# Kernel tuning notes

Hardware: AMD Instinct MI355X
Metric: run time of the kernel (lower is better)

## Reference

```python
import jax, jax.numpy as jnp
import numpy as np

B, P, H, A = 256, 196, 1024, 512

def setup_inputs() -> dict:
    key = jax.random.key(0)
    ks = jax.random.split(key, 20)
    s = 1.0 / np.sqrt(H)
    sa = 1.0 / np.sqrt(A)
    return {
        "spatial_image": jax.random.normal(ks[0], (B, P, H), jnp.float32),
        "decoder_out": jax.random.normal(ks[1], (B, H), jnp.float32),
        "st": jax.random.normal(ks[2], (B, H), jnp.float32),
        "W_sen_aff": jax.random.uniform(ks[3], (H, H), jnp.float32, -s, s),
        "b_sen_aff": jax.random.uniform(ks[4], (H,), jnp.float32, -s, s),
        "W_sen_att": jax.random.uniform(ks[5], (H, A), jnp.float32, -s, s),
        "b_sen_att": jax.random.uniform(ks[6], (A,), jnp.float32, -s, s),
        "W_h_aff": jax.random.uniform(ks[7], (H, H), jnp.float32, -s, s),
        "b_h_aff": jax.random.uniform(ks[8], (H,), jnp.float32, -s, s),
        "W_h_att": jax.random.uniform(ks[9], (H, A), jnp.float32, -s, s),
        "b_h_att": jax.random.uniform(ks[10], (A,), jnp.float32, -s, s),
        "W_v_att": jax.random.uniform(ks[11], (H, A), jnp.float32, -s, s),
        "b_v_att": jax.random.uniform(ks[12], (A,), jnp.float32, -s, s),
        "W_alpha": jax.random.uniform(ks[13], (A, 1), jnp.float32, -sa, sa),
        "b_alpha": jax.random.uniform(ks[14], (1,), jnp.float32, -sa, sa),
        "W_ctx": jax.random.uniform(ks[15], (H, H), jnp.float32, -s, s),
        "b_ctx": jax.random.uniform(ks[16], (H,), jnp.float32, -s, s),
    }

def reference(spatial_image, decoder_out, st,
              W_sen_aff, b_sen_aff, W_sen_att, b_sen_att,
              W_h_aff, b_h_aff, W_h_att, b_h_att,
              W_v_att, b_v_att, W_alpha, b_alpha, W_ctx, b_ctx):
    # visual_attn: [B, P, A]
    visual_attn = jnp.einsum('bph,ha->bpa', spatial_image, W_v_att) + b_v_att
    # sentinel path: [B, H] -> relu affine -> [B, A]
    sentinel_affine = jax.nn.relu(st @ W_sen_aff + b_sen_aff)
    sentinel_attn = sentinel_affine @ W_sen_att + b_sen_att
    # hidden path: [B, H] -> tanh affine -> [B, A]
    hidden_affine = jnp.tanh(decoder_out @ W_h_aff + b_h_aff)
    hidden_attn = hidden_affine @ W_h_att + b_h_att
    # concat sentinel as an extra "pixel": [B, P+1, H] and [B, P+1, A]
    concat_features = jnp.concatenate([spatial_image, sentinel_affine[:, None, :]], axis=1)
    attended_features = jnp.concatenate([visual_attn, sentinel_attn[:, None, :]], axis=1)
    attention = jnp.tanh(attended_features + hidden_attn[:, None, :])  # [B, P+1, A]
    alpha = (jnp.einsum('bpa,ao->bpo', attention, W_alpha) + b_alpha)[..., 0]  # [B, P+1]
    att_weights = jax.nn.softmax(alpha, axis=1)
    context = jnp.einsum('bph,bp->bh', concat_features, att_weights)  # [B, H]
    beta_value = att_weights[:, -1:]  # [B, 1]
    out_l = jnp.tanh((context + hidden_affine) @ W_ctx + b_ctx)  # [B, H]
    return (out_l, att_weights, beta_value)
```

## Files before the change

kernel.cpp:

```cpp
#include <hip/hip_runtime.h>
#include <stdint.h>
#include <stddef.h>

typedef __attribute__((ext_vector_type(4))) float f32x4;
typedef __attribute__((ext_vector_type(8))) short short8;

#define MROWS 50176


static __device__ __forceinline__ int lds_off(int row, int k) {
    int slot = (k >> 3) ^ ((row >> 1) & 3);
    return (row << 6) + (slot << 4) + ((k & 7) << 1);
}

static __device__ __forceinline__ unsigned div196(unsigned g) {
    return (unsigned)(((unsigned long long)g * 85599ull) >> 24);
}

static __device__ __forceinline__ unsigned short f2bf(float f) {
    union { float f; unsigned u; } v; v.f = f;
    unsigned r = v.u + 0x7FFFu + ((v.u >> 16) & 1u);
    return (unsigned short)(r >> 16);
}

static __device__ __forceinline__ unsigned long long pack4bf(f32x4 a) {
    return  (unsigned long long)f2bf(a[0])
         | ((unsigned long long)f2bf(a[1]) << 16)
         | ((unsigned long long)f2bf(a[2]) << 32)
         | ((unsigned long long)f2bf(a[3]) << 48);
}

static __device__ __forceinline__ float tanh_fast(float x) {
    float xc = fminf(fmaxf(x, -9.f), 9.f);
    float e = __builtin_amdgcn_exp2f(xc * 2.885390081777927f);
    return (e - 1.f) * __builtin_amdgcn_rcpf(e + 1.f);
}

static __device__ __forceinline__ void gload_lds16(const void* g, void* l) {
    __builtin_amdgcn_global_load_lds(
        (const __attribute__((address_space(1))) unsigned int*)g,
        (__attribute__((address_space(3))) unsigned int*)l, 16, 0, 0);
}

static __device__ __forceinline__ void kloop_dbuf(
    const float* __restrict__ Abase,
    const unsigned short* __restrict__ Bbase,
    char* sA0, char* sA1, char* sB0, char* sB1,
    f32x4 acc[4][4], int tid)
{
    const int lane = tid & 63, w = tid >> 6;
    const int lrow = lane & 15, lk = lane >> 4;
    const int wr = w >> 1, wc = w & 1;

    const float* Ap[4];
    int aoff[4];
    #pragma unroll
    for (int r = 0; r < 4; ++r) {
        int q = tid + (r << 8);
        int ar = q >> 3, kc = (q & 7) << 2;
        Ap[r] = Abase + (size_t)ar * 1024 + kc;
        aoff[r] = lds_off(ar, kc);
    }
    const unsigned short* Bp[2];
    int bdst[2];
    #pragma unroll
    for (int c = 0; c < 2; ++c) {
        int ch = (w << 1) + c;
        int row = (ch << 4) + (lane >> 2);
        int kg = (lane & 3) ^ ((row >> 1) & 3);
        Bp[c] = Bbase + (size_t)row * 1024 + (kg << 3);
        bdst[c] = ch << 10;
    }

    f32x4 z = {0.f, 0.f, 0.f, 0.f};
    #pragma unroll
    for (int m = 0; m < 4; ++m)
        #pragma unroll
        for (int n = 0; n < 4; ++n) acc[m][n] = z;

    {
        f32x4 a[4];
        #pragma unroll
        for (int r = 0; r < 4; ++r) a[r] = *(const f32x4*)Ap[r];
        #pragma unroll
        for (int c = 0; c < 2; ++c) gload_lds16(Bp[c], sB0 + bdst[c]);
        #pragma unroll
        for (int r = 0; r < 4; ++r)
            *(unsigned long long*)(sA0 + aoff[r]) = pack4bf(a[r]);
    }
    __syncthreads();

    char* sAc = sA0; char* sAn = sA1;
    char* sBc = sB0; char* sBn = sB1;
    for (int ks = 0; ks < 32; ++ks) {
        f32x4 an[4];
        if (ks < 31) {
            const int ko = (ks + 1) << 5;
            #pragma unroll
            for (int r = 0; r < 4; ++r) an[r] = *(const f32x4*)(Ap[r] + ko);
            #pragma unroll
            for (int c = 0; c < 2; ++c) gload_lds16(Bp[c] + ko, sBn + bdst[c]);
        }
        short8 af[4], bf[4];
        #pragma unroll
        for (int m = 0; m < 4; ++m)
            af[m] = *(const short8*)(sAc + lds_off((wr << 6) + (m << 4) + lrow, lk << 3));
        #pragma unroll
        for (int n = 0; n < 4; ++n)
            bf[n] = *(const short8*)(sBc + lds_off((wc << 6) + (n << 4) + lrow, lk << 3));
        #pragma unroll
        for (int m = 0; m < 4; ++m)
            #pragma unroll
            for (int n = 0; n < 4; ++n)
                acc[m][n] = __builtin_amdgcn_mfma_f32_16x16x32_bf16(af[m], bf[n], acc[m][n], 0, 0, 0);
        if (ks < 31) {
            #pragma unroll
            for (int r = 0; r < 4; ++r)
                *(unsigned long long*)(sAn + aoff[r]) = pack4bf(an[r]);
        }
        __syncthreads();
        char* t;
        t = sAc; sAc = sAn; sAn = t;
        t = sBc; sBc = sBn; sBn = t;
    }
}

__global__ __launch_bounds__(256, 4) void attn_alpha_kernel(
    const float* __restrict__ spatial,
    const unsigned short* __restrict__ WvT,
    const float* __restrict__ b_v_att,
    const float* __restrict__ hidden_attn,
    const float* __restrict__ W_alpha,
    float* __restrict__ alphap)
{
    __shared__ char sA[2][8192];
    __shared__ char sB[2][8192];
    __shared__ float alpha_s[128];
    const int tid = threadIdx.x;
    const int n4 = blockIdx.x & 3, mt = blockIdx.x >> 2;
    const int row0 = mt << 7, col0 = n4 << 7;
    if (tid < 128) alpha_s[tid] = 0.f;

    f32x4 acc[4][4];
    kloop_dbuf(spatial + (size_t)row0 * 1024, WvT + (size_t)col0 * 1024,
               sA[0], sA[1], sB[0], sB[1], acc, tid);

    const int lane = tid & 63, w = tid >> 6;
    const int wr = w >> 1, wc = w & 1;
    const int lrow = lane & 15, lk = lane >> 4;

    const unsigned bb0 = div196((unsigned)row0);
    const unsigned bb1 = div196((unsigned)(row0 + 127));
    float bv[4], wa[4], h0[4], h1[4];
    #pragma unroll
    for (int n = 0; n < 4; ++n) {
        int g = col0 + (wc << 6) + (n << 4) + lrow;
        bv[n] = b_v_att[g];
        wa[n] = W_alpha[g];
        h0[n] = hidden_attn[bb0 * 512 + g];
        h1[n] = hidden_attn[bb1 * 512 + g];
    }
    #pragma unroll
    for (int m = 0; m < 4; ++m) {
        #pragma unroll
        for (int i = 0; i < 4; ++i) {
            int rloc = (wr << 6) + (m << 4) + (lk << 2) + i;
            bool first = (div196((unsigned)(row0 + rloc)) == bb0);
            float s = 0.f;
            #pragma unroll
            for (int n = 0; n < 4; ++n) {
                float v = tanh_fast(acc[m][n][i] + bv[n] + (first ? h0[n] : h1[n]));
                s += v * wa[n];
            }
            #pragma unroll
            for (int off = 1; off < 16; off <<= 1) s += __shfl_xor(s, off);
            if (lrow == 0) atomicAdd(&alpha_s[rloc], s);
        }
    }
    __syncthreads();
    if (tid < 128)
        alphap[(size_t)n4 * MROWS + row0 + tid] = alpha_s[tid];
}

struct GemmDesc { const float* A; const unsigned short* BT; const float* bias; float* C; int N; int act; };
struct GemmPair { GemmDesc d[2]; };

__global__ __launch_bounds__(256, 4) void gemm_pair_kernel(GemmPair p)
{
    GemmDesc d = p.d[blockIdx.z];
    __shared__ char sA[2][8192];
    __shared__ char sB[2][8192];
    const int tid = threadIdx.x;
    const int row0 = blockIdx.x << 7;
    const int col0 = blockIdx.y << 7;
    f32x4 acc[4][4];
    kloop_dbuf(d.A + (size_t)row0 * 1024, d.BT + (size_t)col0 * 1024,
               sA[0], sA[1], sB[0], sB[1], acc, tid);
    const int lane = tid & 63, w = tid >> 6;
    const int wr = w >> 1, wc = w & 1;
    const int lrow = lane & 15, lk = lane >> 4;
    #pragma unroll
    for (int n = 0; n < 4; ++n) {
        int col = col0 + (wc << 6) + (n << 4) + lrow;
        float bs = d.bias[col];
        #pragma unroll
        for (int m = 0; m < 4; ++m) {
            int rbase = row0 + (wr << 6) + (m << 4) + (lk << 2);
            #pragma unroll
            for (int i = 0; i < 4; ++i) {
                float v = acc[m][n][i] + bs;
                if (d.act == 1) v = fmaxf(v, 0.f);
                if (d.act == 2) v = tanh_fast(v);
                d.C[(size_t)(rbase + i) * d.N + col] = v;
            }
        }
    }
}

struct TransDesc { const float* src; unsigned short* dst; int K; int N; };
struct TransArgs { TransDesc d[6]; };

__global__ void transpose_cvt_kernel(TransArgs args) {
    TransDesc d = args.d[blockIdx.y];
    int nt = d.N >> 5;
    int tiles = (d.K >> 5) * nt;
    if ((int)blockIdx.x >= tiles) return;
    int tk = blockIdx.x / nt, tn = blockIdx.x % nt;
    __shared__ unsigned short tile[32][33];
    int tx = threadIdx.x & 31, ty = threadIdx.x >> 5;
    int k0 = tk << 5, n0 = tn << 5;
    #pragma unroll
    for (int j = 0; j < 4; ++j)
        tile[ty + j * 8][tx] = f2bf(d.src[(size_t)(k0 + ty + j * 8) * d.N + n0 + tx]);
    __syncthreads();
    #pragma unroll
    for (int j = 0; j < 4; ++j)
        d.dst[(size_t)(n0 + ty + j * 8) * d.K + k0 + tx] = tile[tx][ty + j * 8];
}

__global__ void softmax_sentinel_kernel(
    const float* __restrict__ alphap,
    const float* __restrict__ sen_att, const float* __restrict__ hid_att,
    const float* __restrict__ W_alpha,
    float* __restrict__ att, float* __restrict__ beta)
{
    int b = blockIdx.x, tid = threadIdx.x;
    __shared__ float al[197];
    __shared__ float red[4];
    if (tid < 196) {
        size_t g = (size_t)b * 196 + tid;
        al[tid] = alphap[g] + alphap[MROWS + g] + alphap[2 * MROWS + g] + alphap[3 * MROWS + g];
    }
    float s = 0.f;
    for (int a = tid; a < 512; a += 256)
        s += tanh_fast(sen_att[b * 512 + a] + hid_att[b * 512 + a]) * W_alpha[a];
    #pragma unroll
    for (int off = 1; off < 64; off <<= 1) s += __shfl_xor(s, off);
    if ((tid & 63) == 0) red[tid >> 6] = s;
    __syncthreads();
    if (tid == 0) al[196] = red[0] + red[1] + red[2] + red[3];
    __syncthreads();
    if (tid < 64) {
        float v[4];
        float mx = -1e30f;
        #pragma unroll
        for (int j = 0; j < 4; ++j) {
            int i = tid + j * 64;
            v[j] = (i < 197) ? al[i] : -1e30f;
            mx = fmaxf(mx, v[j]);
        }
        #pragma unroll
        for (int off = 1; off < 64; off <<= 1) mx = fmaxf(mx, __shfl_xor(mx, off));
        float sm = 0.f;
        #pragma unroll
        for (int j = 0; j < 4; ++j) {
            v[j] = __builtin_amdgcn_exp2f((v[j] - mx) * 1.442695040888963f);
            if (tid + j * 64 >= 197) v[j] = 0.f;
            sm += v[j];
        }
        #pragma unroll
        for (int off = 1; off < 64; off <<= 1) sm += __shfl_xor(sm, off);
        float inv = 1.f / sm;
        #pragma unroll
        for (int j = 0; j < 4; ++j) {
            int i = tid + j * 64;
            if (i < 197) {
                float wv = v[j] * inv;
                att[b * 197 + i] = wv;
                if (i == 196) beta[b] = wv;
            }
        }
    }
}

__global__ __launch_bounds__(256) void context_kernel(
    const float* __restrict__ spatial, const float* __restrict__ sen_aff,
    const float* __restrict__ hid_aff, const float* __restrict__ att,
    float* __restrict__ ctxh)
{
    int b = blockIdx.x, half = blockIdx.y, t = threadIdx.x;
    __shared__ float wsm[197];
    if (t < 197) wsm[t] = att[b * 197 + t];
    __syncthreads();
    int h2 = (half << 8) + t;
    const float2* sp = (const float2*)(spatial + (size_t)b * 196 * 1024) + h2;
    float ax = 0.f, ay = 0.f;
    #pragma unroll 4
    for (int p = 0; p < 196; ++p) {
        float2 x = sp[(size_t)p * 512];
        ax += wsm[p] * x.x; ay += wsm[p] * x.y;
    }
    float w196 = wsm[196];
    float2 sa = ((const float2*)(sen_aff + (size_t)b * 1024))[h2];
    float2 ha = ((const float2*)(hid_aff + (size_t)b * 1024))[h2];
    ctxh[(size_t)b * 1024 + 2 * h2]     = ax + w196 * sa.x + ha.x;
    ctxh[(size_t)b * 1024 + 2 * h2 + 1] = ay + w196 * sa.y + ha.y;
}

extern "C" void kernel_launch(void* const* d_in, const int* in_sizes, int n_in,
                              void* d_out, int out_size, void* d_ws, size_t ws_size,
                              hipStream_t stream)
{
    const float* spatial   = (const float*)d_in[0];
    const float* decoder   = (const float*)d_in[1];
    const float* st        = (const float*)d_in[2];
    const float* W_sen_aff = (const float*)d_in[3];
    const float* b_sen_aff = (const float*)d_in[4];
    const float* W_sen_att = (const float*)d_in[5];
    const float* b_sen_att = (const float*)d_in[6];
    const float* W_h_aff   = (const float*)d_in[7];
    const float* b_h_aff   = (const float*)d_in[8];
    const float* W_h_att   = (const float*)d_in[9];
    const float* b_h_att   = (const float*)d_in[10];
    const float* W_v_att   = (const float*)d_in[11];
    const float* b_v_att   = (const float*)d_in[12];
    const float* W_alpha   = (const float*)d_in[13];
    const float* W_ctx     = (const float*)d_in[15];
    const float* b_ctx     = (const float*)d_in[16];

    char* ws = (char*)d_ws;
    size_t off = 0;
    auto alloc = [&](size_t bytes) {
        char* p = ws + off; off += (bytes + 255) & ~(size_t)255; return p;
    };
    unsigned short* WvT  = (unsigned short*)alloc((size_t)512 * 1024 * 2);
    unsigned short* WsaT = (unsigned short*)alloc((size_t)1024 * 1024 * 2);
    unsigned short* WstT = (unsigned short*)alloc((size_t)512 * 1024 * 2);
    unsigned short* WhaT = (unsigned short*)alloc((size_t)1024 * 1024 * 2);
    unsigned short* WhtT = (unsigned short*)alloc((size_t)512 * 1024 * 2);
    unsigned short* WcxT = (unsigned short*)alloc((size_t)1024 * 1024 * 2);
    float* sen_aff = (float*)alloc((size_t)256 * 1024 * 4);
    float* sen_att = (float*)alloc((size_t)256 * 512 * 4);
    float* hid_aff = (float*)alloc((size_t)256 * 1024 * 4);
    float* hid_att = (float*)alloc((size_t)256 * 512 * 4);
    float* alphap  = (float*)alloc((size_t)4 * MROWS * 4);
    float* ctxh    = (float*)alloc((size_t)256 * 1024 * 4);

    float* out_l    = (float*)d_out;
    float* out_att  = out_l + 256 * 1024;
    float* out_beta = out_att + 256 * 197;

    TransArgs ta;
    ta.d[0] = { W_v_att,   WvT,  1024, 512  };
    ta.d[1] = { W_sen_aff, WsaT, 1024, 1024 };
    ta.d[2] = { W_sen_att, WstT, 1024, 512  };
    ta.d[3] = { W_h_aff,   WhaT, 1024, 1024 };
    ta.d[4] = { W_h_att,   WhtT, 1024, 512  };
    ta.d[5] = { W_ctx,     WcxT, 1024, 1024 };
    transpose_cvt_kernel<<<dim3(1024, 6), 256, 0, stream>>>(ta);

    GemmPair p1;
    p1.d[0] = { st,      WsaT, b_sen_aff, sen_aff, 1024, 1 };
    p1.d[1] = { decoder, WhaT, b_h_aff,   hid_aff, 1024, 2 };
    gemm_pair_kernel<<<dim3(2, 8, 2), 256, 0, stream>>>(p1);

    GemmPair p2;
    p2.d[0] = { sen_aff, WstT, b_sen_att, sen_att, 512, 0 };
    p2.d[1] = { hid_aff, WhtT, b_h_att,   hid_att, 512, 0 };
    gemm_pair_kernel<<<dim3(2, 4, 2), 256, 0, stream>>>(p2);

    attn_alpha_kernel<<<1568, 256, 0, stream>>>(spatial, WvT, b_v_att, hid_att, W_alpha, alphap);
    softmax_sentinel_kernel<<<256, 256, 0, stream>>>(alphap, sen_att, hid_att, W_alpha, out_att, out_beta);
    context_kernel<<<dim3(256, 2), 256, 0, stream>>>(spatial, sen_aff, hid_aff, out_att, ctxh);

    GemmPair p3;
    p3.d[0] = { ctxh, WcxT, b_ctx, out_l, 1024, 2 };
    p3.d[1] = { ctxh, WcxT, b_ctx, out_l, 1024, 2 };
    gemm_pair_kernel<<<dim3(2, 8, 1), 256, 0, stream>>>(p3);
}
```

Baseline: 248.2 us.

## Stream GEMM operands directly from global memory into MFMA fragments, dropping LDS staging

Replaces the LDS double-buffered K loop with a loop where each lane loads its A rows (fp32, converted to bf16) and B rows straight from global memory into MFMA fragments. This removes all barriers and LDS traffic. Each block's A/B tiles are re-read by multiple waves through cache instead of being shared via LDS. The change also remaps the block order of the attention GEMM so adjacent blocks are spread across XCDs, lowers launch bounds to 3 blocks per CU, and raises the unroll factor of the context reduction loop. The risk is more global and L2 traffic, plus uncoalesced, strided 32-byte row loads.

```diff
diff --git a/kernel.cpp b/kernel.cpp
--- a/kernel.cpp
+++ b/kernel.cpp
@@ -1,4 +1,5 @@
 #include <hip/hip_runtime.h>
+#include <hip/hip_bf16.h>
 #include <stdint.h>
 #include <stddef.h>
 
@@ -7,11 +8,6 @@
 
 #define MROWS 50176
 
-
-static __device__ __forceinline__ int lds_off(int row, int k) {
-    int slot = (k >> 3) ^ ((row >> 1) & 3);
-    return (row << 6) + (slot << 4) + ((k & 7) << 1);
-}
 
 static __device__ __forceinline__ unsigned div196(unsigned g) {
     return (unsigned)(((unsigned long long)g * 85599ull) >> 24);
@@ -23,54 +19,38 @@
     return (unsigned short)(r >> 16);
 }
 
-static __device__ __forceinline__ unsigned long long pack4bf(f32x4 a) {
-    return  (unsigned long long)f2bf(a[0])
-         | ((unsigned long long)f2bf(a[1]) << 16)
-         | ((unsigned long long)f2bf(a[2]) << 32)
-         | ((unsigned long long)f2bf(a[3]) << 48);
-}
-
 static __device__ __forceinline__ float tanh_fast(float x) {
     float xc = fminf(fmaxf(x, -9.f), 9.f);
     float e = __builtin_amdgcn_exp2f(xc * 2.885390081777927f);
     return (e - 1.f) * __builtin_amdgcn_rcpf(e + 1.f);
 }
 
-static __device__ __forceinline__ void gload_lds16(const void* g, void* l) {
-    __builtin_amdgcn_global_load_lds(
-        (const __attribute__((address_space(1))) unsigned int*)g,
-        (__attribute__((address_space(3))) unsigned int*)l, 16, 0, 0);
-}
-
-static __device__ __forceinline__ void kloop_dbuf(
-    const float* __restrict__ Abase,
-    const unsigned short* __restrict__ Bbase,
-    char* sA0, char* sA1, char* sB0, char* sB1,
+static __device__ __forceinline__ short8 cvt8bf(f32x4 lo, f32x4 hi) {
+    union { short8 s; __hip_bfloat162 h[4]; } u;
+    u.h[0] = __float22bfloat162_rn(make_float2(lo[0], lo[1]));
+    u.h[1] = __float22bfloat162_rn(make_float2(lo[2], lo[3]));
+    u.h[2] = __float22bfloat162_rn(make_float2(hi[0], hi[1]));
+    u.h[3] = __float22bfloat162_rn(make_float2(hi[2], hi[3]));
+    return u.s;
+}
+
+static __device__ __forceinline__ void kloop_stream(
+    const float* __restrict__ A,
+    const unsigned short* __restrict__ B,
     f32x4 acc[4][4], int tid)
 {
     const int lane = tid & 63, w = tid >> 6;
+    const int wr = w >> 1, wc = w & 1;
     const int lrow = lane & 15, lk = lane >> 4;
-    const int wr = w >> 1, wc = w & 1;
 
     const float* Ap[4];
-    int aoff[4];
-    #pragma unroll
-    for (int r = 0; r < 4; ++r) {
-        int q = tid + (r << 8);
-        int ar = q >> 3, kc = (q & 7) << 2;
-        Ap[r] = Abase + (size_t)ar * 1024 + kc;
-        aoff[r] = lds_off(ar, kc);
-    }
-    const unsigned short* Bp[2];
-    int bdst[2];
-    #pragma unroll
-    for (int c = 0; c < 2; ++c) {
-        int ch = (w << 1) + c;
-        int row = (ch << 4) + (lane >> 2);
-        int kg = (lane & 3) ^ ((row >> 1) & 3);
-        Bp[c] = Bbase + (size_t)row * 1024 + (kg << 3);
-        bdst[c] = ch << 10;
-    }
+    const unsigned short* Bp[4];
+    #pragma unroll
+    for (int m = 0; m < 4; ++m)
+        Ap[m] = A + (size_t)((wr << 6) + (m << 4) + lrow) * 1024 + (lk << 3);
+    #pragma unroll
+    for (int n = 0; n < 4; ++n)
+        Bp[n] = B + (size_t)((wc << 6) + (n << 4) + lrow) * 1024 + (lk << 3);
 
     f32x4 z = {0.f, 0.f, 0.f, 0.f};
     #pragma unroll
@@ -78,54 +58,27 @@
         #pragma unroll
         for (int n = 0; n < 4; ++n) acc[m][n] = z;
 
-    {
-        f32x4 a[4];
-        #pragma unroll
-        for (int r = 0; r < 4; ++r) a[r] = *(const f32x4*)Ap[r];
-        #pragma unroll
-        for (int c = 0; c < 2; ++c) gload_lds16(Bp[c], sB0 + bdst[c]);
-        #pragma unroll
-        for (int r = 0; r < 4; ++r)
-            *(unsigned long long*)(sA0 + aoff[r]) = pack4bf(a[r]);
-    }
-    __syncthreads();
-
-    char* sAc = sA0; char* sAn = sA1;
-    char* sBc = sB0; char* sBn = sB1;
+    #pragma unroll 4
     for (int ks = 0; ks < 32; ++ks) {
-        f32x4 an[4];
-        if (ks < 31) {
-            const int ko = (ks + 1) << 5;
-            #pragma unroll
-            for (int r = 0; r < 4; ++r) an[r] = *(const f32x4*)(Ap[r] + ko);
-            #pragma unroll
-            for (int c = 0; c < 2; ++c) gload_lds16(Bp[c] + ko, sBn + bdst[c]);
-        }
         short8 af[4], bf[4];
         #pragma unroll
-        for (int m = 0; m < 4; ++m)
-            af[m] = *(const short8*)(sAc + lds_off((wr << 6) + (m << 4) + lrow, lk << 3));
+        for (int m = 0; m < 4; ++m) {
+            f32x4 lo = *(const f32x4*)(Ap[m] + (ks << 5));
+            f32x4 hi = *(const f32x4*)(Ap[m] + (ks << 5) + 4);
+            af[m] = cvt8bf(lo, hi);
+        }
         #pragma unroll
         for (int n = 0; n < 4; ++n)
-            bf[n] = *(const short8*)(sBc + lds_off((wc << 6) + (n << 4) + lrow, lk << 3));
+            bf[n] = *(const short8*)(Bp[n] + (ks << 5));
         #pragma unroll
         for (int m = 0; m < 4; ++m)
             #pragma unroll
             for (int n = 0; n < 4; ++n)
                 acc[m][n] = __builtin_amdgcn_mfma_f32_16x16x32_bf16(af[m], bf[n], acc[m][n], 0, 0, 0);
-        if (ks < 31) {
-            #pragma unroll
-            for (int r = 0; r < 4; ++r)
-                *(unsigned long long*)(sAn + aoff[r]) = pack4bf(an[r]);
-        }
-        __syncthreads();
-        char* t;
-        t = sAc; sAc = sAn; sAn = t;
-        t = sBc; sBc = sBn; sBn = t;
-    }
-}
-
-__global__ __launch_bounds__(256, 4) void attn_alpha_kernel(
+    }
+}
+
+__global__ __launch_bounds__(256, 3) void attn_alpha_kernel(
     const float* __restrict__ spatial,
     const unsigned short* __restrict__ WvT,
     const float* __restrict__ b_v_att,
@@ -133,17 +86,17 @@
     const float* __restrict__ W_alpha,
     float* __restrict__ alphap)
 {
-    __shared__ char sA[2][8192];
-    __shared__ char sB[2][8192];
     __shared__ float alpha_s[128];
     const int tid = threadIdx.x;
-    const int n4 = blockIdx.x & 3, mt = blockIdx.x >> 2;
+    const int j = blockIdx.x;
+    const int wk = (j & 7) * 196 + (j >> 3);
+    const int mt = wk >> 2, n4 = wk & 3;
     const int row0 = mt << 7, col0 = n4 << 7;
     if (tid < 128) alpha_s[tid] = 0.f;
+    __syncthreads();
 
     f32x4 acc[4][4];
-    kloop_dbuf(spatial + (size_t)row0 * 1024, WvT + (size_t)col0 * 1024,
-               sA[0], sA[1], sB[0], sB[1], acc, tid);
+    kloop_stream(spatial + (size_t)row0 * 1024, WvT + (size_t)col0 * 1024, acc, tid);
 
     const int lane = tid & 63, w = tid >> 6;
     const int wr = w >> 1, wc = w & 1;
@@ -185,17 +138,14 @@
 struct GemmDesc { const float* A; const unsigned short* BT; const float* bias; float* C; int N; int act; };
 struct GemmPair { GemmDesc d[2]; };
 
-__global__ __launch_bounds__(256, 4) void gemm_pair_kernel(GemmPair p)
+__global__ __launch_bounds__(256, 3) void gemm_pair_kernel(GemmPair p)
 {
     GemmDesc d = p.d[blockIdx.z];
-    __shared__ char sA[2][8192];
-    __shared__ char sB[2][8192];
     const int tid = threadIdx.x;
     const int row0 = blockIdx.x << 7;
     const int col0 = blockIdx.y << 7;
     f32x4 acc[4][4];
-    kloop_dbuf(d.A + (size_t)row0 * 1024, d.BT + (size_t)col0 * 1024,
-               sA[0], sA[1], sB[0], sB[1], acc, tid);
+    kloop_stream(d.A + (size_t)row0 * 1024, d.BT + (size_t)col0 * 1024, acc, tid);
     const int lane = tid & 63, w = tid >> 6;
     const int wr = w >> 1, wc = w & 1;
     const int lrow = lane & 15, lk = lane >> 4;
@@ -264,28 +214,28 @@
         float v[4];
         float mx = -1e30f;
         #pragma unroll
-        for (int j = 0; j < 4; ++j) {
-            int i = tid + j * 64;
-            v[j] = (i < 197) ? al[i] : -1e30f;
-            mx = fmaxf(mx, v[j]);
+        for (int jj = 0; jj < 4; ++jj) {
+            int i = tid + jj * 64;
+            v[jj] = (i < 197) ? al[i] : -1e30f;
+            mx = fmaxf(mx, v[jj]);
         }
         #pragma unroll
         for (int off = 1; off < 64; off <<= 1) mx = fmaxf(mx, __shfl_xor(mx, off));
         float sm = 0.f;
         #pragma unroll
-        for (int j = 0; j < 4; ++j) {
-            v[j] = __builtin_amdgcn_exp2f((v[j] - mx) * 1.442695040888963f);
-            if (tid + j * 64 >= 197) v[j] = 0.f;
-            sm += v[j];
+        for (int jj = 0; jj < 4; ++jj) {
+            v[jj] = __builtin_amdgcn_exp2f((v[jj] - mx) * 1.442695040888963f);
+            if (tid + jj * 64 >= 197) v[jj] = 0.f;
+            sm += v[jj];
         }
         #pragma unroll
         for (int off = 1; off < 64; off <<= 1) sm += __shfl_xor(sm, off);
         float inv = 1.f / sm;
         #pragma unroll
-        for (int j = 0; j < 4; ++j) {
-            int i = tid + j * 64;
+        for (int jj = 0; jj < 4; ++jj) {
+            int i = tid + jj * 64;
             if (i < 197) {
-                float wv = v[j] * inv;
+                float wv = v[jj] * inv;
                 att[b * 197 + i] = wv;
                 if (i == 196) beta[b] = wv;
             }
@@ -305,7 +255,7 @@
     int h2 = (half << 8) + t;
     const float2* sp = (const float2*)(spatial + (size_t)b * 196 * 1024) + h2;
     float ax = 0.f, ay = 0.f;
-    #pragma unroll 4
+    #pragma unroll 8
     for (int p = 0; p < 196; ++p) {
         float2 x = sp[(size_t)p * 512];
         ax += wsm[p] * x.x; ay += wsm[p] * x.y;
```

Result: slower. 544.2 us (+119.3%).
